# Kernel tuning notes

Measured on AMD Instinct MI355X. Metric: run time of the kernel, lower is better.

Reference implementation:

```python
import jax, jax.numpy as jnp
import numpy as np

DIM = 2048
NUM_HEADS = 16
NUM_KV_HEADS = 4
HEAD_DIM = DIM // NUM_HEADS          # 128
GROUP = NUM_HEADS // NUM_KV_HEADS    # 4
ROPE_DIMS = 32                       # partial RoPE: rope_dims < head_dim
ROPE_BASE = 10000.0
QK_GAIN_INIT = 5.0
LOGIT_SOFTCAP = 30.0
BATCH = 2
SEQLEN = 2048


def setup_inputs() -> dict:
    key = jax.random.key(0)
    ks = jax.random.split(key, 5)
    x = jax.random.normal(ks[0], (BATCH, SEQLEN, DIM), dtype=jnp.float32)
    s = 0.02
    Wq = jax.random.normal(ks[1], (DIM, DIM), dtype=jnp.float32) * s
    Wk = jax.random.normal(ks[2], (NUM_KV_HEADS * HEAD_DIM, DIM), dtype=jnp.float32) * s
    Wv = jax.random.normal(ks[3], (NUM_KV_HEADS * HEAD_DIM, DIM), dtype=jnp.float32) * s
    Wproj = jax.random.normal(ks[4], (DIM, DIM), dtype=jnp.float32) * s
    q_gain = jnp.full((NUM_HEADS,), QK_GAIN_INIT, dtype=jnp.float32)
    return {"x": x, "Wq": Wq, "Wk": Wk, "Wv": Wv, "Wproj": Wproj, "q_gain": q_gain}


def _rms_norm(t):
    # torch F.rms_norm with no weight: x / sqrt(mean(x^2) + eps)
    eps = jnp.finfo(t.dtype).eps
    return t * jax.lax.rsqrt(jnp.mean(t * t, axis=-1, keepdims=True) + eps)


def _rope_tables(seqlen, dtype):
    inv_freq = 1.0 / (ROPE_BASE ** (jnp.arange(0, ROPE_DIMS, 2, dtype=jnp.float32) / ROPE_DIMS))
    t = jnp.arange(seqlen, dtype=jnp.float32)
    freqs = jnp.outer(t, inv_freq)  # [S, ROPE_DIMS/2]
    return jnp.cos(freqs).astype(dtype), jnp.sin(freqs).astype(dtype)


def _apply_rotary(x, cos, sin):
    # x: [B, S, H, D]; cos/sin: [S, rd/2]; partial rope on first rd dims
    rd = cos.shape[-1] * 2
    c = cos[None, :, None, :]
    s = sin[None, :, None, :]
    x_rope, x_pass = x[..., :rd], x[..., rd:]
    half = rd // 2
    x1, x2 = x_rope[..., :half], x_rope[..., half:]
    x_rot = jnp.concatenate((x1 * c + x2 * s, -x1 * s + x2 * c), axis=-1)
    return jnp.concatenate((x_rot, x_pass), axis=-1)


def reference(x, Wq, Wk, Wv, Wproj, q_gain):
    B, S, D = x.shape
    q = (x @ Wq.T).reshape(B, S, NUM_HEADS, HEAD_DIM)
    k = (x @ Wk.T).reshape(B, S, NUM_KV_HEADS, HEAD_DIM)
    v = (x @ Wv.T).reshape(B, S, NUM_KV_HEADS, HEAD_DIM)

    q = _rms_norm(q)
    k = _rms_norm(k)

    cos, sin = _rope_tables(S, q.dtype)
    q = _apply_rotary(q, cos, sin)
    k = _apply_rotary(k, cos, sin)

    q = q * q_gain.astype(q.dtype)[None, None, :, None]

    # GQA causal attention with logit softcap; SDPA default scale 1/sqrt(head_dim)
    scale = 1.0 / np.sqrt(HEAD_DIM)
    qg = q.reshape(B, S, NUM_KV_HEADS, GROUP, HEAD_DIM)
    scores = jnp.einsum('bqhgd,bkhd->bhgqk', qg, k) * scale  # [B,Hkv,G,S,S]
    scores = LOGIT_SOFTCAP * jnp.tanh(scores / LOGIT_SOFTCAP)
    causal = jnp.tril(jnp.ones((S, S), dtype=bool))
    scores = jnp.where(causal[None, None, None], scores, -jnp.inf)
    attn = jax.nn.softmax(scores, axis=-1)
    y = jnp.einsum('bhgqk,bkhd->bqhgd', attn, v)  # [B,S,Hkv,G,D]
    y = y.reshape(B, S, NUM_HEADS * HEAD_DIM)

    return y @ Wproj.T
```

## Files before the change

kernel.cpp:

```cpp
#include <hip/hip_runtime.h>
#include <type_traits>

#define BATCH 2
#define S_LEN 2048
#define DIM 2048
#define NH 16
#define NKV 4
#define HD 128

typedef _Float16 f16x8 __attribute__((ext_vector_type(8)));
typedef float f32x4 __attribute__((ext_vector_type(4)));
typedef unsigned int u32x4 __attribute__((ext_vector_type(4)));
typedef unsigned short u16x4 __attribute__((ext_vector_type(4)));
typedef unsigned short u16x8 __attribute__((ext_vector_type(8)));

__device__ __forceinline__ unsigned short f2h_bits(float f) {
  _Float16 h = (_Float16)f;
  return __builtin_bit_cast(unsigned short, h);
}
__device__ __forceinline__ float h2f(unsigned short u) {
  return (float)__builtin_bit_cast(_Float16, u);
}
__device__ __forceinline__ f16x8 ld8(const unsigned short* p) {
  u32x4 v = *reinterpret_cast<const u32x4*>(p);
  return __builtin_bit_cast(f16x8, v);
}
__device__ __forceinline__ void gload_lds16(const unsigned short* g, unsigned short* l) {
  __builtin_amdgcn_global_load_lds(
      (const __attribute__((address_space(1))) unsigned int*)g,
      (__attribute__((address_space(3))) unsigned int*)l, 16, 0, 0);
}

#define VMWAIT(n) asm volatile("s_waitcnt vmcnt(" #n ")" ::: "memory")

__global__ __launch_bounds__(256) void cvt_all(const float* __restrict__ x,
                                               const float* __restrict__ Wq,
                                               const float* __restrict__ Wk,
                                               const float* __restrict__ Wv,
                                               const float* __restrict__ Wp,
                                               unsigned short* __restrict__ xb,
                                               unsigned short* __restrict__ wqkv,
                                               unsigned short* __restrict__ wpj) {
  int i = blockIdx.x * 256 + threadIdx.x;
  const float* src;
  unsigned short* dst;
  if (i < 2097152) {
    src = x + (long)i * 4; dst = xb + (long)i * 4;
  } else if (i < 3145728) {
    int k = i - 2097152; src = Wq + (long)k * 4; dst = wqkv + (long)k * 4;
  } else if (i < 3407872) {
    int k = i - 3145728; src = Wk + (long)k * 4; dst = wqkv + 4194304 + (long)k * 4;
  } else if (i < 3670016) {
    int k = i - 3407872; src = Wv + (long)k * 4; dst = wqkv + 5242880 + (long)k * 4;
  } else {
    int k = i - 3670016; src = Wp + (long)k * 4; dst = wpj + (long)k * 4;
  }
  f32x4 v = *reinterpret_cast<const f32x4*>(src);
  u16x4 o;
  o.x = f2h_bits(v.x); o.y = f2h_bits(v.y); o.z = f2h_bits(v.z); o.w = f2h_bits(v.w);
  *reinterpret_cast<u16x4*>(dst) = o;
}

__global__ __launch_bounds__(256) void rope_tables(float* __restrict__ c, float* __restrict__ s) {
  int idx = blockIdx.x * 256 + threadIdx.x;
  if (idx >= S_LEN * 16) return;
  int i = idx & 15, t = idx >> 4;
  float inv = exp2f(-(float)i * (13.287712379549449f / 16.0f));
  float f = (float)t * inv;
  c[idx] = cosf(f);
  s[idx] = sinf(f);
}

template <int NREP, typename OUT>
__global__ __launch_bounds__(512, 2) void gemm_pl(const unsigned short* __restrict__ A,
                                                  const unsigned short* __restrict__ B,
                                                  OUT* __restrict__ C, int K, int ldc) {
  constexpr int BN = 64 * NREP;
  constexpr int BSH = BN * 32;
  constexpr int TS = 16384 + 2 * BSH;
  __shared__ unsigned short lds[2][TS];
  const int tid = threadIdx.x, lane = tid & 63;
  const int wm = tid >> 8, wn = (tid >> 6) & 3;
  const int rlo = lane & 15, hi = lane >> 4;
  const int m0 = blockIdx.x * 256, n0 = blockIdx.y * BN;
  const int NT = K >> 6;
  const int brow = wn * (16 * NREP);
  const int sA_s = tid >> 2;
  const int pc2 = tid & 3;

  auto aRow = [&](int sig) { return (sig & 63) + ((sig >> 6) & 1) * 128 + (sig >> 7) * 64; };

  auto stageAll = [&](int slot, int k0) {
#pragma unroll
    for (int kk = 0; kk < 2; ++kk)
#pragma unroll
      for (int sh = 0; sh < 2; ++sh) {
        int sig = sh * 128 + sA_s;
        int r = aRow(sig);
        int lc2 = pc2 ^ (sig & 3);
        gload_lds16(A + (long)(m0 + r) * K + k0 + kk * 32 + lc2 * 8,
                    &lds[slot][kk * 8192 + sh * 4096 + tid * 8]);
      }
#pragma unroll
    for (int kk = 0; kk < 2; ++kk)
#pragma unroll
      for (int q = 0; q < (NREP + 1) / 2; ++q) {
        int idx = (q == 0) ? tid : (512 + (tid & 255));
        int r = idx >> 2;
        int lc2 = (idx & 3) ^ (r & 3);
        gload_lds16(B + (long)(n0 + r) * K + k0 + kk * 32 + lc2 * 8,
                    &lds[slot][16384 + kk * BSH + idx * 8]);
      }
  };

  f32x4 acc[8][NREP] = {};

  auto rdA = [&](const unsigned short* As, int kk, int mh, f16x8* af) {
#pragma unroll
    for (int i = 0; i < 4; ++i) {
      int ms = mh * 4 + i;
      int sig = (ms & 3) * 16 + rlo + wm * 64 + (ms >> 2) * 128;
      af[i] = ld8(&As[kk * 8192 + sig * 32 + ((hi ^ (sig & 3)) * 8)]);
    }
  };
  auto rdB = [&](const unsigned short* Bs, int kk, f16x8* bf) {
#pragma unroll
    for (int j = 0; j < NREP; ++j) {
      int r = brow + j * 16 + rlo;
      bf[j] = ld8(&Bs[kk * BSH + r * 32 + ((hi ^ (r & 3)) * 8)]);
    }
  };
  auto mm = [&](const f16x8* af, const f16x8* bf, int mh) {
    __builtin_amdgcn_s_setprio(1);
#pragma unroll
    for (int i = 0; i < 4; ++i)
#pragma unroll
      for (int j = 0; j < NREP; ++j)
        acc[mh * 4 + i][j] =
            __builtin_amdgcn_mfma_f32_16x16x32_f16(af[i], bf[j], acc[mh * 4 + i][j], 0, 0, 0);
    __builtin_amdgcn_s_setprio(0);
  };

  stageAll(0, 0);
  for (int t = 0; t < NT; ++t) {
    const int slot = t & 1;
    const unsigned short* As = &lds[slot][0];
    const unsigned short* Bs = &lds[slot][16384];
    VMWAIT(0);
    __builtin_amdgcn_s_barrier();
    asm volatile("" ::: "memory");
    if (t + 1 < NT) stageAll(slot ^ 1, (t + 1) << 6);
    f16x8 bf0[NREP], bf1[NREP], afE[4], afO[4];
    rdB(Bs, 0, bf0);
    rdA(As, 0, 0, afE);
    rdB(Bs, 1, bf1);
    rdA(As, 1, 0, afO);
    mm(afE, bf0, 0);
    rdA(As, 0, 1, afE);
    mm(afO, bf1, 0);
    rdA(As, 1, 1, afO);
    mm(afE, bf0, 1);
    mm(afO, bf1, 1);
  }

#pragma unroll
  for (int ms = 0; ms < 8; ++ms)
#pragma unroll
    for (int j = 0; j < NREP; ++j) {
      int row = m0 + wm * 128 + ms * 16 + hi * 4;
      int col = n0 + brow + j * 16 + rlo;
#pragma unroll
      for (int r = 0; r < 4; ++r) {
        float v = acc[ms][j][r];
        if constexpr (std::is_same<OUT, float>::value)
          C[(long)(row + r) * ldc + col] = v;
        else
          C[(long)(row + r) * ldc + col] = f2h_bits(v);
      }
    }
}

__global__ __launch_bounds__(256) void qknorm_rope(const unsigned short* __restrict__ qkv,
                                                   const float* __restrict__ ctab,
                                                   const float* __restrict__ stab,
                                                   const float* __restrict__ qgain,
                                                   unsigned short* __restrict__ Qb,
                                                   unsigned short* __restrict__ Kb) {
  const int lane = threadIdx.x & 63;
  const int row = blockIdx.x * 4 + (threadIdx.x >> 6);
  const int NQROWS = BATCH * S_LEN * NH;
  const unsigned short* src;
  unsigned short* dst;
  int m, hh;
  bool isQ;
  if (row < NQROWS) {
    m = row >> 4; hh = row & 15;
    src = qkv + (long)m * 3072 + hh * HD;
    int b = m >> 11, s = m & (S_LEN - 1);
    dst = Qb + (((long)(b * NH + hh)) * S_LEN + s) * HD;
    isQ = true;
  } else {
    int rk = row - NQROWS;
    m = rk >> 2; hh = rk & 3;
    src = qkv + (long)m * 3072 + 2048 + hh * HD;
    int b = m >> 11, s = m & (S_LEN - 1);
    dst = Kb + (((long)(b * NKV + hh)) * S_LEN + s) * HD;
    isQ = false;
  }
  const int s = m & (S_LEN - 1);
  float x0 = h2f(src[lane]);
  float x1 = h2f(src[lane + 64]);
  float ss = x0 * x0 + x1 * x1;
  ss += __shfl_xor(ss, 1); ss += __shfl_xor(ss, 2); ss += __shfl_xor(ss, 4);
  ss += __shfl_xor(ss, 8); ss += __shfl_xor(ss, 16); ss += __shfl_xor(ss, 32);
  float rn = rsqrtf(ss * (1.0f / 128.0f) + 1.1920929e-07f);
  float n0 = x0 * rn, n1 = x1 * rn;
  float partner = __shfl_xor(n0, 16);
  if (lane < 32) {
    int i = lane & 15;
    float c = ctab[s * 16 + i], sn = stab[s * 16 + i];
    n0 = (lane < 16) ? (n0 * c + partner * sn) : (n0 * c - partner * sn);
  }
  if (isQ) { float g = qgain[hh]; n0 *= g; n1 *= g; }
  dst[lane] = f2h_bits(n0);
  dst[lane + 64] = f2h_bits(n1);
}

__global__ __launch_bounds__(256) void vtrans(const unsigned short* __restrict__ qkv,
                                              unsigned short* __restrict__ Vt) {
  int idx = blockIdx.x * 256 + threadIdx.x;
  int d = idx & 127;
  int sc = (idx >> 7) & 255;
  int kvh = (idx >> 15) & 3;
  int b = idx >> 17;
  u16x8 v;
#pragma unroll
  for (int j = 0; j < 8; ++j)
    v[j] = qkv[((long)(b * S_LEN + sc * 8 + j)) * 3072 + 2560 + kvh * HD + d];
  *reinterpret_cast<u16x8*>(Vt + (((long)(b * NKV + kvh)) * HD + d) * S_LEN + sc * 8) = v;
}

#define ATT_C3 ((float)(0.08838834764831845 * (2.0 / 30.0) * 1.4426950408889634))
#define ATT_C4 ((float)(30.0 * 1.4426950408889634))
#define ATT_C5 ((float)(60.0 * 1.4426950408889634))
#define ATT_THR ((float)(8.0 * 1.4426950408889634))

__global__ __launch_bounds__(256, 4) void attn(const unsigned short* __restrict__ Qb,
                                               const unsigned short* __restrict__ Kb,
                                               const unsigned short* __restrict__ Vt,
                                               unsigned short* __restrict__ Yb) {
  __shared__ unsigned short sm[2][8192];
  const int tid = threadIdx.x, wid = tid >> 6, lane = tid & 63;
  const int gx = blockIdx.x;
  const int qq = gx >> 8;
  const int a = (gx >> 5) & 7;
  const int h = gx & 15, b = (gx >> 4) & 1;
  int qb;
  if (qq == 0) qb = 31 - a;
  else if (qq == 1) qb = 16 + a;
  else if (qq == 2) qb = 15 - a;
  else qb = a;

  const int kvh = h >> 2;
  const int rlo = lane & 15, hi = lane >> 4;
  const int q0 = qb * 64 + wid * 16;
  const unsigned short* Kp = Kb + ((long)(b * NKV + kvh)) * S_LEN * HD;
  const unsigned short* Vp = Vt + ((long)(b * NKV + kvh)) * HD * S_LEN;
  const unsigned short* Qp = Qb + (((long)(b * NH + h)) * S_LEN + q0) * HD;
  f16x8 bq[4];
#pragma unroll
  for (int dk = 0; dk < 4; ++dk) bq[dk] = ld8(Qp + rlo * HD + dk * 32 + hi * 8);

  const int kx = rlo & 7;
  const int vx = hi ^ ((rlo >> 1) & 3);
  const unsigned short* aK[4];
#pragma unroll
  for (int dk = 0; dk < 4; ++dk) aK[dk] = &sm[0][rlo * 128 + ((dk * 4 + hi) ^ kx) * 8];
  const unsigned short* aV = &sm[0][4096 + rlo * 32 + vx * 8];

  const int i0 = tid, i1 = tid + 256;
  const int rho0 = i0 >> 4, rho1 = i1 >> 4;
  auto kvperm = [](int r) { return 8 * ((r >> 2) & 3) + (r & 3) + 4 * (r >> 4); };
  const unsigned short* sK0 = Kp + (long)kvperm(rho0) * HD + ((i0 & 15) ^ (rho0 & 7)) * 8;
  const unsigned short* sK1 = Kp + (long)kvperm(rho1) * HD + ((i1 & 15) ^ (rho1 & 7)) * 8;
  const int vd0 = i0 >> 2, vd1 = i1 >> 2;
  const unsigned short* sV0 = Vp + (long)vd0 * S_LEN + ((i0 & 3) ^ ((vd0 >> 1) & 3)) * 8;
  const unsigned short* sV1 = Vp + (long)vd1 * S_LEN + ((i1 & 3) ^ ((vd1 >> 1) & 3)) * 8;
  unsigned short* dK0 = &sm[0][rho0 * 128 + (i0 & 15) * 8];
  unsigned short* dK1 = &sm[0][rho1 * 128 + (i1 & 15) * 8];
  unsigned short* dV0 = &sm[0][4096 + vd0 * 32 + (i0 & 3) * 8];
  unsigned short* dV1 = &sm[0][4096 + vd1 * 32 + (i1 & 3) * 8];

  f32x4 acc[8] = {};
  float m2c = ATT_C4 + 128.0f;
  float l_run = 0.0f;
  const int nt = 2 * qb + 2;
  const int twlast = 2 * qb + (wid >> 1);

#define STAGE(SLOT)                                                       \
  {                                                                       \
    gload_lds16(sK0, dK0 + (SLOT)*8192);                                  \
    gload_lds16(sK1, dK1 + (SLOT)*8192);                                  \
    gload_lds16(sV0, dV0 + (SLOT)*8192);                                  \
    gload_lds16(sV1, dV1 + (SLOT)*8192);                                  \
    sK0 += 4096; sK1 += 4096; sV0 += 32; sV1 += 32;                       \
  }

#define COMPUTE(T, SLOT)                                                              \
  {                                                                                   \
    f16x8 ka0[4], ka1[4];                                                             \
    _Pragma("unroll")                                                                 \
    for (int dk = 0; dk < 4; ++dk) {                                                  \
      ka0[dk] = ld8(aK[dk] + (SLOT)*8192);                                            \
      ka1[dk] = ld8(aK[dk] + (SLOT)*8192 + 2048);                                     \
    }                                                                                 \
    f32x4 s0 = {0.f, 0.f, 0.f, 0.f}, s1 = s0;                                         \
    __builtin_amdgcn_s_setprio(1);                                                    \
    _Pragma("unroll")                                                                 \
    for (int dk = 0; dk < 4; ++dk) {                                                  \
      s0 = __builtin_amdgcn_mfma_f32_16x16x32_f16(ka0[dk], bq[dk], s0, 0, 0, 0);      \
      s1 = __builtin_amdgcn_mfma_f32_16x16x32_f16(ka1[dk], bq[dk], s1, 0, 0, 0);      \
    }                                                                                 \
    __builtin_amdgcn_s_setprio(0);                                                    \
    float ea[8];                                                                      \
    _Pragma("unroll")                                                                 \
    for (int jj = 0; jj < 8; ++jj) {                                                  \
      float sc = (jj < 4) ? s0[jj] : s1[jj - 4];                                      \
      float u = __builtin_amdgcn_exp2f(sc * ATT_C3);                                  \
      float rr = __builtin_amdgcn_rcpf(u + 1.0f);                                     \
      ea[jj] = fmaf(-ATT_C5, rr, m2c);                                                \
    }                                                                                 \
    if ((T) == twlast) {                                                              \
      int qrel = q0 + rlo - 32 * (T);                                                 \
      _Pragma("unroll")                                                               \
      for (int jj = 0; jj < 8; ++jj)                                                  \
        ea[jj] = (8 * hi + jj > qrel) ? -1e30f : ea[jj];                              \
    }                                                                                 \
    float pm = ea[0];                                                                 \
    _Pragma("unroll")                                                                 \
    for (int jj = 1; jj < 8; ++jj) pm = fmaxf(pm, ea[jj]);                            \
    if (!__all(pm <= ATT_THR)) {                                                      \
      float red = fmaxf(pm, __shfl_xor(pm, 16));                                      \
      red = fmaxf(red, __shfl_xor(red, 32));                                          \
      red = fmaxf(red, 0.0f);                                                         \
      m2c -= red;                                                                     \
      float ff = __builtin_amdgcn_exp2f(-red);                                        \
      l_run *= ff;                                                                    \
      _Pragma("unroll")                                                               \
      for (int dt = 0; dt < 8; ++dt) acc[dt] *= ff;                                   \
      _Pragma("unroll")                                                               \
      for (int jj = 0; jj < 8; ++jj) ea[jj] -= red;                                   \
    }                                                                                 \
    float pv[8];                                                                      \
    _Pragma("unroll")                                                                 \
    for (int jj = 0; jj < 8; ++jj) pv[jj] = __builtin_amdgcn_exp2f(ea[jj]);           \
    l_run += ((pv[0] + pv[1]) + (pv[2] + pv[3])) + ((pv[4] + pv[5]) + (pv[6] + pv[7]));\
    u32x4 pk;                                                                         \
    pk.x = __builtin_bit_cast(unsigned int, __builtin_amdgcn_cvt_pkrtz(pv[0], pv[1]));\
    pk.y = __builtin_bit_cast(unsigned int, __builtin_amdgcn_cvt_pkrtz(pv[2], pv[3]));\
    pk.z = __builtin_bit_cast(unsigned int, __builtin_amdgcn_cvt_pkrtz(pv[4], pv[5]));\
    pk.w = __builtin_bit_cast(unsigned int, __builtin_amdgcn_cvt_pkrtz(pv[6], pv[7]));\
    f16x8 bp = __builtin_bit_cast(f16x8, pk);                                         \
    __builtin_amdgcn_s_setprio(1);                                                    \
    _Pragma("unroll")                                                                 \
    for (int g = 0; g < 2; ++g) {                                                     \
      f16x8 av[4];                                                                    \
      _Pragma("unroll")                                                               \
      for (int i = 0; i < 4; ++i) av[i] = ld8(aV + (SLOT)*8192 + (g * 4 + i) * 512);  \
      _Pragma("unroll")                                                               \
      for (int i = 0; i < 4; ++i)                                                     \
        acc[g * 4 + i] =                                                              \
            __builtin_amdgcn_mfma_f32_16x16x32_f16(av[i], bp, acc[g * 4 + i], 0, 0, 0);\
    }                                                                                 \
    __builtin_amdgcn_s_setprio(0);                                                    \
  }

  STAGE(0);
  for (int t = 0; t < nt; t += 2) {
    VMWAIT(0);
    __builtin_amdgcn_s_barrier();
    asm volatile("" ::: "memory");
    STAGE(1);
    if (t <= twlast) COMPUTE(t, 0);
    VMWAIT(0);
    __builtin_amdgcn_s_barrier();
    asm volatile("" ::: "memory");
    if (t + 2 < nt) STAGE(0);
    if (t + 1 <= twlast) COMPUTE(t + 1, 1);
  }
#undef STAGE
#undef COMPUTE

  float l = l_run + __shfl_xor(l_run, 16);
  l += __shfl_xor(l, 32);
  float inv = 1.0f / l;
  unsigned short* yp = Yb + ((long)(b * S_LEN + q0 + rlo)) * DIM + h * HD + 4 * hi;
#pragma unroll
  for (int dt = 0; dt < 8; ++dt) {
    u16x4 o;
#pragma unroll
    for (int r = 0; r < 4; ++r) o[r] = f2h_bits(acc[dt][r] * inv);
    *reinterpret_cast<u16x4*>(yp + dt * 16) = o;
  }
}

extern "C" void kernel_launch(void* const* d_in, const int* in_sizes, int n_in,
                              void* d_out, int out_size, void* d_ws, size_t ws_size,
                              hipStream_t stream) {
  const float* x = (const float*)d_in[0];
  const float* Wq = (const float*)d_in[1];
  const float* Wk = (const float*)d_in[2];
  const float* Wv = (const float*)d_in[3];
  const float* Wp = (const float*)d_in[4];
  const float* qg = (const float*)d_in[5];
  float* out = (float*)d_out;

  char* ws = (char*)d_ws;
  size_t off = 0;
  auto alloc = [&](size_t bytes) {
    char* p = ws + off;
    off += (bytes + 255) & ~(size_t)255;
    return p;
  };
  unsigned short* xb   = (unsigned short*)alloc(8388608ull * 2);
  unsigned short* wqkv = (unsigned short*)alloc(6291456ull * 2);
  unsigned short* wpj  = (unsigned short*)alloc(4194304ull * 2);
  unsigned short* qkv  = (unsigned short*)alloc(4096ull * 3072 * 2);
  unsigned short* Qbuf = (unsigned short*)alloc(8388608ull * 2);
  unsigned short* Kb   = (unsigned short*)alloc(2097152ull * 2);
  unsigned short* Vt   = (unsigned short*)alloc(2097152ull * 2);
  unsigned short* Yb   = (unsigned short*)alloc(8388608ull * 2);
  float* ctab = (float*)alloc(32768ull * 4);
  float* stab = (float*)alloc(32768ull * 4);

  cvt_all<<<18432, 256, 0, stream>>>(x, Wq, Wk, Wv, Wp, xb, wqkv, wpj);
  rope_tables<<<128, 256, 0, stream>>>(ctab, stab);

  gemm_pl<3, unsigned short><<<dim3(16, 16), 512, 0, stream>>>(xb, wqkv, qkv, 2048, 3072);

  qknorm_rope<<<(BATCH * S_LEN * (NH + NKV)) / 4, 256, 0, stream>>>(qkv, ctab, stab, qg, Qbuf, Kb);
  vtrans<<<(BATCH * NKV * HD * (S_LEN / 8)) / 256, 256, 0, stream>>>(qkv, Vt);

  attn<<<1024, 256, 0, stream>>>(Qbuf, Kb, Vt, Yb);

  gemm_pl<2, float><<<dim3(16, 16), 512, 0, stream>>>(Yb, wpj, out, 2048, 2048);
}
```

Baseline: 199.9 us.

## Switch GEMM to 4-slot LDS ring with prefetch depth two

Restructures the fp16 MFMA GEMM main loop from a double-buffered 64-wide K step into a 4-slot ring of 32-wide K steps, staging two tiles ahead and waiting only on older vmcnt groups instead of draining all loads. Global pointers are precomputed and incremented, and the LDS swizzle changes to use (row>>1)&3. The intent is to hide global-load latency better and cut address arithmetic, at the cost of twice as many barriers per K and less MFMA work between syncs.

After: 195.8 us. -2.1%, faster.

```diff
diff --git a/kernel.cpp b/kernel.cpp
--- a/kernel.cpp
+++ b/kernel.cpp
@@ -77,57 +77,52 @@
                                                   OUT* __restrict__ C, int K, int ldc) {
   constexpr int BN = 64 * NREP;
   constexpr int BSH = BN * 32;
-  constexpr int TS = 16384 + 2 * BSH;
-  __shared__ unsigned short lds[2][TS];
+  constexpr int TS = 8192 + BSH;
+  __shared__ unsigned short lds[4][TS];
   const int tid = threadIdx.x, lane = tid & 63;
   const int wm = tid >> 8, wn = (tid >> 6) & 3;
   const int rlo = lane & 15, hi = lane >> 4;
   const int m0 = blockIdx.x * 256, n0 = blockIdx.y * BN;
-  const int NT = K >> 6;
+  const int NT = K >> 5;
   const int brow = wn * (16 * NREP);
-  const int sA_s = tid >> 2;
-  const int pc2 = tid & 3;
 
   auto aRow = [&](int sig) { return (sig & 63) + ((sig >> 6) & 1) * 128 + (sig >> 7) * 64; };
 
-  auto stageAll = [&](int slot, int k0) {
-#pragma unroll
-    for (int kk = 0; kk < 2; ++kk)
-#pragma unroll
-      for (int sh = 0; sh < 2; ++sh) {
-        int sig = sh * 128 + sA_s;
-        int r = aRow(sig);
-        int lc2 = pc2 ^ (sig & 3);
-        gload_lds16(A + (long)(m0 + r) * K + k0 + kk * 32 + lc2 * 8,
-                    &lds[slot][kk * 8192 + sh * 4096 + tid * 8]);
-      }
-#pragma unroll
-    for (int kk = 0; kk < 2; ++kk)
-#pragma unroll
-      for (int q = 0; q < (NREP + 1) / 2; ++q) {
-        int idx = (q == 0) ? tid : (512 + (tid & 255));
-        int r = idx >> 2;
-        int lc2 = (idx & 3) ^ (r & 3);
-        gload_lds16(B + (long)(n0 + r) * K + k0 + kk * 32 + lc2 * 8,
-                    &lds[slot][16384 + kk * BSH + idx * 8]);
-      }
+  const int sigA0 = tid >> 2, sigA1 = 128 + (tid >> 2);
+  const unsigned short* pA0 =
+      A + (long)(m0 + aRow(sigA0)) * K + (((tid & 3) ^ ((sigA0 >> 1) & 3)) * 8);
+  const unsigned short* pA1 =
+      A + (long)(m0 + aRow(sigA1)) * K + (((tid & 3) ^ ((sigA1 >> 1) & 3)) * 8);
+  const int rB0 = tid >> 2;
+  const unsigned short* pB0 = B + (long)(n0 + rB0) * K + (((tid & 3) ^ ((rB0 >> 1) & 3)) * 8);
+  const int idx1 = 512 + (tid & 255);
+  const int rB1 = idx1 >> 2;
+  const unsigned short* pB1 = B + (long)(n0 + rB1) * K + (((idx1 & 3) ^ ((rB1 >> 1) & 3)) * 8);
+
+  auto stage = [&](int slot) {
+    gload_lds16(pA0, &lds[slot][tid * 8]);
+    gload_lds16(pA1, &lds[slot][4096 + tid * 8]);
+    gload_lds16(pB0, &lds[slot][8192 + tid * 8]);
+    if constexpr (NREP == 3) gload_lds16(pB1, &lds[slot][8192 + idx1 * 8]);
+    pA0 += 32; pA1 += 32; pB0 += 32;
+    if constexpr (NREP == 3) pB1 += 32;
   };
 
   f32x4 acc[8][NREP] = {};
 
-  auto rdA = [&](const unsigned short* As, int kk, int mh, f16x8* af) {
+  auto rdA = [&](const unsigned short* As, int mh, f16x8* af) {
 #pragma unroll
     for (int i = 0; i < 4; ++i) {
       int ms = mh * 4 + i;
       int sig = (ms & 3) * 16 + rlo + wm * 64 + (ms >> 2) * 128;
-      af[i] = ld8(&As[kk * 8192 + sig * 32 + ((hi ^ (sig & 3)) * 8)]);
+      af[i] = ld8(&As[sig * 32 + ((hi ^ ((sig >> 1) & 3)) * 8)]);
     }
   };
-  auto rdB = [&](const unsigned short* Bs, int kk, f16x8* bf) {
+  auto rdB = [&](const unsigned short* Bs, f16x8* bf) {
 #pragma unroll
     for (int j = 0; j < NREP; ++j) {
       int r = brow + j * 16 + rlo;
-      bf[j] = ld8(&Bs[kk * BSH + r * 32 + ((hi ^ (r & 3)) * 8)]);
+      bf[j] = ld8(&Bs[r * 32 + ((hi ^ ((r >> 1) & 3)) * 8)]);
     }
   };
   auto mm = [&](const f16x8* af, const f16x8* bf, int mh) {
@@ -141,26 +136,26 @@
     __builtin_amdgcn_s_setprio(0);
   };
 
-  stageAll(0, 0);
+  stage(0);
+  stage(1);
   for (int t = 0; t < NT; ++t) {
-    const int slot = t & 1;
-    const unsigned short* As = &lds[slot][0];
-    const unsigned short* Bs = &lds[slot][16384];
-    VMWAIT(0);
+    const int slot = t & 3;
+    if (t == NT - 1) {
+      VMWAIT(0);
+    } else {
+      if constexpr (NREP == 3) VMWAIT(4); else VMWAIT(3);
+    }
     __builtin_amdgcn_s_barrier();
     asm volatile("" ::: "memory");
-    if (t + 1 < NT) stageAll(slot ^ 1, (t + 1) << 6);
-    f16x8 bf0[NREP], bf1[NREP], afE[4], afO[4];
-    rdB(Bs, 0, bf0);
-    rdA(As, 0, 0, afE);
-    rdB(Bs, 1, bf1);
-    rdA(As, 1, 0, afO);
-    mm(afE, bf0, 0);
-    rdA(As, 0, 1, afE);
-    mm(afO, bf1, 0);
-    rdA(As, 1, 1, afO);
-    mm(afE, bf0, 1);
-    mm(afO, bf1, 1);
+    if (t + 2 < NT) stage((t + 2) & 3);
+    const unsigned short* As = &lds[slot][0];
+    const unsigned short* Bs = &lds[slot][8192];
+    f16x8 bf[NREP], af0[4], af1[4];
+    rdB(Bs, bf);
+    rdA(As, 0, af0);
+    rdA(As, 1, af1);
+    mm(af0, bf, 0);
+    mm(af1, bf, 1);
   }
 
 #pragma unroll
```

## Split GEMM prefetch into staged halves with partial waits and reorder attention blocks

Applied to the files above, without the earlier changes.

The GEMM main loop is restructured into four phases with barriers between them. The next tile's global-to-LDS loads are issued in two halves, and the loop waits only on the older outstanding loads (partial vmcnt) rather than draining all of them, to overlap memory with MFMA work. The loads now use precomputed, incrementing source pointers and a changed LDS swizzle ((row>>1)&3). The attention grid mapping is also reordered so that blocks sharing a KV head are adjacent, which is meant to improve L2 reuse of K/V. In exchange, the GEMM now has more barriers per iteration and more fragile wait-count bookkeeping.

New measurement: 200.8 us. No clear change (+0.4%).

```diff
diff --git a/kernel.cpp b/kernel.cpp
--- a/kernel.cpp
+++ b/kernel.cpp
@@ -72,12 +72,11 @@
 }
 
 template <int NREP, typename OUT>
-__global__ __launch_bounds__(512, 2) void gemm_pl(const unsigned short* __restrict__ A,
-                                                  const unsigned short* __restrict__ B,
-                                                  OUT* __restrict__ C, int K, int ldc) {
+__global__ __launch_bounds__(512, 2) void gemm8(const unsigned short* __restrict__ A,
+                                                const unsigned short* __restrict__ B,
+                                                OUT* __restrict__ C, int K, int ldc) {
   constexpr int BN = 64 * NREP;
-  constexpr int BSH = BN * 32;
-  constexpr int TS = 16384 + 2 * BSH;
+  constexpr int TS = 16384 + BN * 64;
   __shared__ unsigned short lds[2][TS];
   const int tid = threadIdx.x, lane = tid & 63;
   const int wm = tid >> 8, wn = (tid >> 6) & 3;
@@ -85,82 +84,98 @@
   const int m0 = blockIdx.x * 256, n0 = blockIdx.y * BN;
   const int NT = K >> 6;
   const int brow = wn * (16 * NREP);
-  const int sA_s = tid >> 2;
-  const int pc2 = tid & 3;
-
-  auto aRow = [&](int sig) { return (sig & 63) + ((sig >> 6) & 1) * 128 + (sig >> 7) * 64; };
-
-  auto stageAll = [&](int slot, int k0) {
-#pragma unroll
-    for (int kk = 0; kk < 2; ++kk)
-#pragma unroll
-      for (int sh = 0; sh < 2; ++sh) {
-        int sig = sh * 128 + sA_s;
-        int r = aRow(sig);
-        int lc2 = pc2 ^ (sig & 3);
-        gload_lds16(A + (long)(m0 + r) * K + k0 + kk * 32 + lc2 * 8,
-                    &lds[slot][kk * 8192 + sh * 4096 + tid * 8]);
-      }
-#pragma unroll
-    for (int kk = 0; kk < 2; ++kk)
-#pragma unroll
-      for (int q = 0; q < (NREP + 1) / 2; ++q) {
-        int idx = (q == 0) ? tid : (512 + (tid & 255));
-        int r = idx >> 2;
-        int lc2 = (idx & 3) ^ (r & 3);
-        gload_lds16(B + (long)(n0 + r) * K + k0 + kk * 32 + lc2 * 8,
-                    &lds[slot][16384 + kk * BSH + idx * 8]);
-      }
+
+  auto asrc = [&](int c) {
+    int flat = c * 512 + tid;
+    int kk = flat >> 10, row = (flat >> 2) & 255, gr = flat & 3;
+    return A + (long)(m0 + row) * K + kk * 32 + ((gr ^ ((row >> 1) & 3)) * 8);
+  };
+  auto bsrc = [&](int c) {
+    int flat = c * 512 + tid;
+    int kk = flat / (BN * 4), rem = flat % (BN * 4);
+    int r = rem >> 2, gr = rem & 3;
+    return B + (long)(n0 + r) * K + kk * 32 + ((gr ^ ((r >> 1) & 3)) * 8);
+  };
+  const unsigned short* pA0 = asrc(0);
+  const unsigned short* pA1 = asrc(1);
+  const unsigned short* pA2 = asrc(2);
+  const unsigned short* pA3 = asrc(3);
+  const unsigned short* pB0 = bsrc(0);
+  const unsigned short* pB1 = bsrc(1);
+  const unsigned short* pB2 = (NREP == 3) ? bsrc(2) : nullptr;
+
+  auto stG0 = [&](int slot) {
+    gload_lds16(pA0, &lds[slot][(0 * 512 + tid) * 8]);
+    gload_lds16(pA1, &lds[slot][(1 * 512 + tid) * 8]);
+    gload_lds16(pB0, &lds[slot][16384 + (0 * 512 + tid) * 8]);
+    if constexpr (NREP == 3) gload_lds16(pB1, &lds[slot][16384 + (1 * 512 + tid) * 8]);
+    pA0 += 64; pA1 += 64; pB0 += 64;
+    if constexpr (NREP == 3) pB1 += 64;
+  };
+  auto stG1 = [&](int slot) {
+    gload_lds16(pA2, &lds[slot][(2 * 512 + tid) * 8]);
+    gload_lds16(pA3, &lds[slot][(3 * 512 + tid) * 8]);
+    if constexpr (NREP == 3) {
+      gload_lds16(pB2, &lds[slot][16384 + (2 * 512 + tid) * 8]);
+      pB2 += 64;
+    } else {
+      gload_lds16(pB1, &lds[slot][16384 + (1 * 512 + tid) * 8]);
+      pB1 += 64;
+    }
+    pA2 += 64; pA3 += 64;
   };
 
   f32x4 acc[8][NREP] = {};
 
-  auto rdA = [&](const unsigned short* As, int kk, int mh, f16x8* af) {
+  auto phase = [&](const unsigned short* As, const unsigned short* Bs, int MH, int KK) {
+    f16x8 af[4], bf[NREP];
 #pragma unroll
     for (int i = 0; i < 4; ++i) {
-      int ms = mh * 4 + i;
-      int sig = (ms & 3) * 16 + rlo + wm * 64 + (ms >> 2) * 128;
-      af[i] = ld8(&As[kk * 8192 + sig * 32 + ((hi ^ (sig & 3)) * 8)]);
+      int row = wm * 128 + (MH * 4 + i) * 16 + rlo;
+      af[i] = ld8(&As[KK * 8192 + row * 32 + ((hi ^ ((row >> 1) & 3)) * 8)]);
     }
-  };
-  auto rdB = [&](const unsigned short* Bs, int kk, f16x8* bf) {
 #pragma unroll
     for (int j = 0; j < NREP; ++j) {
       int r = brow + j * 16 + rlo;
-      bf[j] = ld8(&Bs[kk * BSH + r * 32 + ((hi ^ (r & 3)) * 8)]);
+      bf[j] = ld8(&Bs[KK * (BN * 32) + r * 32 + ((hi ^ ((r >> 1) & 3)) * 8)]);
     }
-  };
-  auto mm = [&](const f16x8* af, const f16x8* bf, int mh) {
     __builtin_amdgcn_s_setprio(1);
 #pragma unroll
     for (int i = 0; i < 4; ++i)
 #pragma unroll
       for (int j = 0; j < NREP; ++j)
-        acc[mh * 4 + i][j] =
-            __builtin_amdgcn_mfma_f32_16x16x32_f16(af[i], bf[j], acc[mh * 4 + i][j], 0, 0, 0);
+        acc[MH * 4 + i][j] =
+            __builtin_amdgcn_mfma_f32_16x16x32_f16(af[i], bf[j], acc[MH * 4 + i][j], 0, 0, 0);
     __builtin_amdgcn_s_setprio(0);
   };
 
-  stageAll(0, 0);
+  stG0(0);
+  stG1(0);
   for (int t = 0; t < NT; ++t) {
     const int slot = t & 1;
     const unsigned short* As = &lds[slot][0];
     const unsigned short* Bs = &lds[slot][16384];
-    VMWAIT(0);
-    __builtin_amdgcn_s_barrier();
-    asm volatile("" ::: "memory");
-    if (t + 1 < NT) stageAll(slot ^ 1, (t + 1) << 6);
-    f16x8 bf0[NREP], bf1[NREP], afE[4], afO[4];
-    rdB(Bs, 0, bf0);
-    rdA(As, 0, 0, afE);
-    rdB(Bs, 1, bf1);
-    rdA(As, 1, 0, afO);
-    mm(afE, bf0, 0);
-    rdA(As, 0, 1, afE);
-    mm(afO, bf1, 0);
-    rdA(As, 1, 1, afO);
-    mm(afE, bf0, 1);
-    mm(afO, bf1, 1);
+    const bool pf = (t + 1) < NT;
+    VMWAIT(3);
+    __builtin_amdgcn_s_barrier();
+    asm volatile("" ::: "memory");
+    if (pf) stG0(slot ^ 1);
+    phase(As, Bs, 0, 0);
+    __builtin_amdgcn_s_barrier();
+    asm volatile("" ::: "memory");
+    if (pf) stG1(slot ^ 1);
+    phase(As, Bs, 1, 0);
+    if (pf) {
+      if constexpr (NREP == 3) VMWAIT(7); else VMWAIT(6);
+    } else {
+      VMWAIT(0);
+    }
+    __builtin_amdgcn_s_barrier();
+    asm volatile("" ::: "memory");
+    phase(As, Bs, 0, 1);
+    __builtin_amdgcn_s_barrier();
+    asm volatile("" ::: "memory");
+    phase(As, Bs, 1, 1);
   }
 
 #pragma unroll
@@ -252,16 +267,15 @@
   __shared__ unsigned short sm[2][8192];
   const int tid = threadIdx.x, wid = tid >> 6, lane = tid & 63;
   const int gx = blockIdx.x;
-  const int qq = gx >> 8;
-  const int a = (gx >> 5) & 7;
-  const int h = gx & 15, b = (gx >> 4) & 1;
+  const int kvh = gx & 3, b = (gx >> 2) & 1, hh = (gx >> 3) & 3;
+  const int h = kvh * 4 + hh;
+  const int a = (gx >> 5) & 7, qq = gx >> 8;
   int qb;
   if (qq == 0) qb = 31 - a;
   else if (qq == 1) qb = 16 + a;
   else if (qq == 2) qb = 15 - a;
   else qb = a;
 
-  const int kvh = h >> 2;
   const int rlo = lane & 15, hi = lane >> 4;
   const int q0 = qb * 64 + wid * 16;
   const unsigned short* Kp = Kb + ((long)(b * NKV + kvh)) * S_LEN * HD;
@@ -436,12 +450,12 @@
   cvt_all<<<18432, 256, 0, stream>>>(x, Wq, Wk, Wv, Wp, xb, wqkv, wpj);
   rope_tables<<<128, 256, 0, stream>>>(ctab, stab);
 
-  gemm_pl<3, unsigned short><<<dim3(16, 16), 512, 0, stream>>>(xb, wqkv, qkv, 2048, 3072);
+  gemm8<3, unsigned short><<<dim3(16, 16), 512, 0, stream>>>(xb, wqkv, qkv, 2048, 3072);
 
   qknorm_rope<<<(BATCH * S_LEN * (NH + NKV)) / 4, 256, 0, stream>>>(qkv, ctab, stab, qg, Qbuf, Kb);
   vtrans<<<(BATCH * NKV * HD * (S_LEN / 8)) / 256, 256, 0, stream>>>(qkv, Vt);
 
   attn<<<1024, 256, 0, stream>>>(Qbuf, Kb, Vt, Yb);
 
-  gemm_pl<2, float><<<dim3(16, 16), 512, 0, stream>>>(Yb, wpj, out, 2048, 2048);
-}
+  gemm8<2, float><<<dim3(16, 16), 512, 0, stream>>>(Yb, wpj, out, 2048, 2048);
+}
```
